# Optimization experiments

Measured on AMD Instinct MI355X. Metric: run time of the kernel, lower is better.

Reference implementation:

```python
import jax, jax.numpy as jnp
import numpy as np

N = 100000   # nodes
E = 600000   # edges
G = 4096     # graphs in batch
D_IN = 73
D_E = 101
D = 128      # latent_dim
BN_EPS = 1e-5


def _bn(h, gamma, beta):
    # BatchNorm1d in training mode: batch statistics (biased variance)
    m = h.mean(axis=0)
    v = h.var(axis=0)
    return (h - m) * jax.lax.rsqrt(v + BN_EPS) * gamma + beta


def setup_inputs() -> dict:
    key = jax.random.key(0)
    ks = jax.random.split(key, 24)
    inp = {
        "x": jax.random.normal(ks[0], (N, D_IN), jnp.float32),
        "edge_attr": jax.random.normal(ks[1], (E, D_E), jnp.float32),
        "src": jax.random.randint(ks[2], (E,), 0, N, jnp.int32),
        "dst": jax.random.randint(ks[3], (E,), 0, N, jnp.int32),
        "batch": jnp.sort(jax.random.randint(ks[4], (N,), 0, G, jnp.int32)),
        # node embedding Linear(73 -> 128)
        "W_emb": jax.random.normal(ks[5], (D_IN, D), jnp.float32) / np.sqrt(D_IN),
        "b_emb": jnp.zeros((D,), jnp.float32),
    }
    k = 6
    for i in range(2):
        inp[f"We{i}"] = jax.random.normal(ks[k], (D_E, D), jnp.float32) / np.sqrt(D_E); k += 1
        inp[f"be{i}"] = jnp.zeros((D,), jnp.float32)
        inp[f"W1_{i}"] = jax.random.normal(ks[k], (D, 2 * D), jnp.float32) / np.sqrt(D); k += 1
        inp[f"b1_{i}"] = jnp.zeros((2 * D,), jnp.float32)
        inp[f"g1_{i}"] = jnp.ones((2 * D,), jnp.float32)
        inp[f"bb1_{i}"] = jnp.zeros((2 * D,), jnp.float32)
        inp[f"W2_{i}"] = jax.random.normal(ks[k], (2 * D, D), jnp.float32) / np.sqrt(2 * D); k += 1
        inp[f"b2_{i}"] = jnp.zeros((D,), jnp.float32)
        inp[f"go_{i}"] = jnp.ones((D,), jnp.float32)
        inp[f"bo_{i}"] = jnp.zeros((D,), jnp.float32)
    return inp


def _forward(x, edge_attr, src, dst, batch,
             W_emb, b_emb,
             We0, be0, W1_0, b1_0, g1_0, bb1_0, W2_0, b2_0, go_0, bo_0,
             We1, be1, W1_1, b1_1, g1_1, bb1_1, W2_1, b2_1, go_1, bo_1):
    layers = [
        (We0, be0, W1_0, b1_0, g1_0, bb1_0, W2_0, b2_0, go_0, bo_0),
        (We1, be1, W1_1, b1_1, g1_1, bb1_1, W2_1, b2_1, go_1, bo_1),
    ]
    h = x @ W_emb + b_emb  # [N, D]
    n_layers = len(layers)
    for i, (We, be, W1, b1, g1, bb1, W2, b2, go, bo) in enumerate(layers):
        e = edge_attr @ We + be                         # [E, D]
        msg = jax.nn.relu(h[src] + e)                   # gather + add + ReLU
        agg = jax.ops.segment_sum(msg, dst, num_segments=N)  # scatter-sum
        z = h + agg                                     # (1 + eps) * x_i + aggr, eps = 0
        z = jax.nn.relu(_bn(z @ W1 + b1, g1, bb1))      # MLP: Linear -> BN -> ReLU
        h = _bn(z @ W2 + b2, go, bo)                    # Linear -> outer BN
        if i != n_layers - 1:
            h = jax.nn.relu(h)
        # dropout p=0 -> identity
    # global mean pool over graphs
    sums = jax.ops.segment_sum(h, batch, num_segments=G)            # [G, D]
    counts = jax.ops.segment_sum(jnp.ones((h.shape[0],), h.dtype), batch, num_segments=G)
    return sums / jnp.maximum(counts, 1.0)[:, None]


def reference(x, edge_attr, src, dst, batch,
              W_emb, b_emb,
              We0, be0, W1_0, b1_0, g1_0, bb1_0, W2_0, b2_0, go_0, bo_0,
              We1, be1, W1_1, b1_1, g1_1, bb1_1, W2_1, b2_1, go_1, bo_1):
    return _forward(x, edge_attr, src, dst, batch, W_emb, b_emb,
                    We0, be0, W1_0, b1_0, g1_0, bb1_0, W2_0, b2_0, go_0, bo_0,
                    We1, be1, W1_1, b1_1, g1_1, bb1_1, W2_1, b2_1, go_1, bo_1)
```

## Files before the change

### kernel.cpp

```cpp
#include <hip/hip_runtime.h>
#include <cstddef>

#define NN  100000
#define NE  600000
#define NG  4096
#define DIN 73
#define DE  101
#define DD  128
#define DD2 256
#define NP  100096
#define EP  600064

typedef unsigned int uint;
typedef unsigned short ushort;
typedef __attribute__((ext_vector_type(8))) short bf16x8;
typedef __attribute__((ext_vector_type(4))) float f32x4;

__device__ __forceinline__ void fadd_atomic(float* p, float v) { unsafeAtomicAdd(p, v); }

__device__ __forceinline__ ushort f2bf(float f) {
    uint u = __float_as_uint(f);
    uint r = (u + 0x7fffu + ((u >> 16) & 1u)) >> 16;
    return (ushort)r;
}
__device__ __forceinline__ float bf2f(ushort u) { return __uint_as_float(((uint)u) << 16); }


__global__ void hist_kernel(const int* __restrict__ dst, int* __restrict__ deg) {
    int e = blockIdx.x * blockDim.x + threadIdx.x;
    if (e < NE) atomicAdd(&deg[dst[e]], 1);
}

__global__ __launch_bounds__(256) void scan_chunk_kernel(
    const int* __restrict__ deg, int* __restrict__ offs, int* __restrict__ csums)
{
    const int b = blockIdx.x, t = threadIdx.x;
    const int base = b * 1024 + t * 4;
    int v[4];
    #pragma unroll
    for (int i = 0; i < 4; ++i) v[i] = (base + i < NN) ? deg[base + i] : 0;
    int tsum = v[0] + v[1] + v[2] + v[3];
    const int lane = t & 63, w = t >> 6;
    int x = tsum;
    #pragma unroll
    for (int d = 1; d < 64; d <<= 1) {
        int y = __shfl_up(x, d, 64);
        if (lane >= d) x += y;
    }
    __shared__ int wsum[4];
    if (lane == 63) wsum[w] = x;
    __syncthreads();
    int woff = 0;
    for (int i = 0; i < w; ++i) woff += wsum[i];
    int run = woff + x - tsum;
    #pragma unroll
    for (int i = 0; i < 4; ++i) {
        if (base + i < NN) offs[base + i] = run;
        run += v[i];
    }
    if (t == 255) csums[b] = woff + x;
}

__global__ void scan_tops_kernel(int* __restrict__ csums, int* __restrict__ offs, int nchunks) {
    if (threadIdx.x == 0 && blockIdx.x == 0) {
        int run = 0;
        for (int i = 0; i < nchunks; ++i) { int c = csums[i]; csums[i] = run; run += c; }
        offs[NN] = run;
    }
}

__global__ void scan_add_kernel(int* __restrict__ offs, const int* __restrict__ csums) {
    int i = blockIdx.x * blockDim.x + threadIdx.x;
    if (i < NN) offs[i] += csums[i >> 10];
}

__global__ void scatter_kernel(const int* __restrict__ dst, const int* __restrict__ src,
                               const int* __restrict__ offs, int* __restrict__ cursor,
                               int* __restrict__ eperm, int* __restrict__ srcp)
{
    int e = blockIdx.x * blockDim.x + threadIdx.x;
    if (e >= NE) return;
    int d = dst[e];
    int pos = offs[d] + atomicAdd(&cursor[d], 1);
    eperm[e] = pos;
    srcp[pos] = src[e];
}

__global__ void gstart_kernel(const int* __restrict__ batch, int* __restrict__ gstart) {
    int n = blockIdx.x * blockDim.x + threadIdx.x;
    if (n > NN) return;
    if (n == NN) {
        for (int g = batch[NN - 1] + 1; g <= NG; ++g) gstart[g] = NN;
        return;
    }
    int b = batch[n];
    int pb = (n == 0) ? -1 : batch[n - 1];
    for (int g = pb + 1; g <= b; ++g) gstart[g] = n;
}


__global__ __launch_bounds__(256) void cvt_ea_kernel(const float* __restrict__ ea,
                                                     const int* __restrict__ eperm,
                                                     ushort* __restrict__ eabc)
{
    const int t = threadIdx.x;
    const int r = blockIdx.x * 8 + (t >> 5);
    if (r >= NE) return;
    const int pos = eperm[r];
    const int c = (t & 31) * 4;
    ushort4 o;
    #pragma unroll
    for (int i = 0; i < 4; ++i) {
        const int col = c + i;
        float v = (col < DE) ? ea[(size_t)r * DE + col] : ((col == DE) ? 1.0f : 0.0f);
        ((ushort*)&o)[i] = f2bf(v);
    }
    *(ushort4*)&eabc[(size_t)pos * 128 + c] = o;
}

__global__ void cvt_wt_kernel(const float* __restrict__ in, ushort* __restrict__ out,
                              int Kin, int Nn, int Kp, const float* __restrict__ bias)
{
    const int n = blockIdx.x;
    for (int k = threadIdx.x; k < Kp; k += blockDim.x) {
        float v = 0.0f;
        if (k < Kin) v = in[(size_t)k * Nn + n];
        else if (k == Kin && bias) v = bias[n];
        out[(size_t)n * Kp + k] = f2bf(v);
    }
}


__global__ __launch_bounds__(256, 2) void edge_gemm_kernel(
    const ushort* __restrict__ eab, const ushort* __restrict__ Wt,
    ushort* __restrict__ ecsr)
{
    const int wid = threadIdx.x >> 6;
    const int msub = wid >> 1, nsl = wid & 1;
    const int lane = threadIdx.x & 63, l15 = lane & 15, grp = lane >> 4;
    const int n0 = nsl * 64;
    bf16x8 A[4][4];
    #pragma unroll
    for (int nf = 0; nf < 4; ++nf)
        #pragma unroll
        for (int kk = 0; kk < 4; ++kk)
            A[nf][kk] = *(const bf16x8*)(Wt + (size_t)(n0 + nf * 16 + l15) * 128 + kk * 32 + grp * 8);

    const int ntiles = EP / 128;
    for (int t = blockIdx.x; t < ntiles; t += gridDim.x) {
        const int m0 = t * 128 + msub * 64;
        f32x4 acc[4][4];
        #pragma unroll
        for (int i = 0; i < 4; ++i)
            #pragma unroll
            for (int j = 0; j < 4; ++j) acc[i][j] = (f32x4){0.f, 0.f, 0.f, 0.f};
        #pragma unroll
        for (int kk = 0; kk < 4; ++kk) {
            bf16x8 b[4];
            #pragma unroll
            for (int mf = 0; mf < 4; ++mf)
                b[mf] = *(const bf16x8*)(eab + (size_t)(m0 + mf * 16 + l15) * 128 + kk * 32 + grp * 8);
            #pragma unroll
            for (int mf = 0; mf < 4; ++mf)
                #pragma unroll
                for (int nf = 0; nf < 4; ++nf)
                    acc[mf][nf] = __builtin_amdgcn_mfma_f32_16x16x32_bf16(A[nf][kk], b[mf], acc[mf][nf], 0, 0, 0);
        }
        #pragma unroll
        for (int mf = 0; mf < 4; ++mf) {
            ushort* rp = &ecsr[(size_t)(m0 + mf * 16 + l15) * 128 + n0];
            #pragma unroll
            for (int nf = 0; nf < 4; ++nf) {
                ushort4 o;
                o.x = f2bf(acc[mf][nf][0]);
                o.y = f2bf(acc[mf][nf][1]);
                o.z = f2bf(acc[mf][nf][2]);
                o.w = f2bf(acc[mf][nf][3]);
                *(ushort4*)&rp[nf * 16 + grp * 4] = o;
            }
        }
    }
}

__global__ __launch_bounds__(256, 2) void mlp1_gemm_kernel(
    const ushort* __restrict__ z, const ushort* __restrict__ Wt,
    const float* __restrict__ bias, ushort* __restrict__ y)
{
    const int n0 = (threadIdx.x >> 6) * 64;
    const int lane = threadIdx.x & 63, l15 = lane & 15, grp = lane >> 4;
    bf16x8 A[4][4];
    #pragma unroll
    for (int nf = 0; nf < 4; ++nf)
        #pragma unroll
        for (int kk = 0; kk < 4; ++kk)
            A[nf][kk] = *(const bf16x8*)(Wt + (size_t)(n0 + nf * 16 + l15) * 128 + kk * 32 + grp * 8);
    float4 bv[4];
    #pragma unroll
    for (int nf = 0; nf < 4; ++nf) bv[nf] = *(const float4*)&bias[n0 + nf * 16 + grp * 4];

    const int ntiles = NP / 64;
    for (int t = blockIdx.x; t < ntiles; t += gridDim.x) {
        const int m0 = t * 64;
        f32x4 acc[4][4];
        #pragma unroll
        for (int i = 0; i < 4; ++i)
            #pragma unroll
            for (int j = 0; j < 4; ++j) acc[i][j] = (f32x4){0.f, 0.f, 0.f, 0.f};
        #pragma unroll
        for (int kk = 0; kk < 4; ++kk) {
            bf16x8 b[4];
            #pragma unroll
            for (int mf = 0; mf < 4; ++mf)
                b[mf] = *(const bf16x8*)(z + (size_t)(m0 + mf * 16 + l15) * 128 + kk * 32 + grp * 8);
            #pragma unroll
            for (int mf = 0; mf < 4; ++mf)
                #pragma unroll
                for (int nf = 0; nf < 4; ++nf)
                    acc[mf][nf] = __builtin_amdgcn_mfma_f32_16x16x32_bf16(A[nf][kk], b[mf], acc[mf][nf], 0, 0, 0);
        }
        #pragma unroll
        for (int mf = 0; mf < 4; ++mf) {
            ushort* rp = &y[(size_t)(m0 + mf * 16 + l15) * 256 + n0];
            #pragma unroll
            for (int nf = 0; nf < 4; ++nf) {
                ushort4 o;
                o.x = f2bf(acc[mf][nf][0] + bv[nf].x);
                o.y = f2bf(acc[mf][nf][1] + bv[nf].y);
                o.z = f2bf(acc[mf][nf][2] + bv[nf].z);
                o.w = f2bf(acc[mf][nf][3] + bv[nf].w);
                *(ushort4*)&rp[nf * 16 + grp * 4] = o;
            }
        }
    }
}

__global__ __launch_bounds__(256, 2) void mlp2_gemm_kernel(
    const ushort* __restrict__ y1, const ushort* __restrict__ Wt,
    const float* __restrict__ bias, ushort* __restrict__ y2)
{
    const int wid = threadIdx.x >> 6;
    const int msub = wid >> 1, nsl = wid & 1;
    const int lane = threadIdx.x & 63, l15 = lane & 15, grp = lane >> 4;
    const int n0 = nsl * 64;
    bf16x8 A[4][8];
    #pragma unroll
    for (int nf = 0; nf < 4; ++nf)
        #pragma unroll
        for (int kk = 0; kk < 8; ++kk)
            A[nf][kk] = *(const bf16x8*)(Wt + (size_t)(n0 + nf * 16 + l15) * 256 + kk * 32 + grp * 8);
    float4 bv[4];
    #pragma unroll
    for (int nf = 0; nf < 4; ++nf) bv[nf] = *(const float4*)&bias[n0 + nf * 16 + grp * 4];

    const int ntiles = NP / 128;
    for (int t = blockIdx.x; t < ntiles; t += gridDim.x) {
        const int m0 = t * 128 + msub * 64;
        f32x4 acc[4][4];
        #pragma unroll
        for (int i = 0; i < 4; ++i)
            #pragma unroll
            for (int j = 0; j < 4; ++j) acc[i][j] = (f32x4){0.f, 0.f, 0.f, 0.f};
        #pragma unroll
        for (int kk = 0; kk < 8; ++kk) {
            bf16x8 b[4];
            #pragma unroll
            for (int mf = 0; mf < 4; ++mf)
                b[mf] = *(const bf16x8*)(y1 + (size_t)(m0 + mf * 16 + l15) * 256 + kk * 32 + grp * 8);
            #pragma unroll
            for (int mf = 0; mf < 4; ++mf)
                #pragma unroll
                for (int nf = 0; nf < 4; ++nf)
                    acc[mf][nf] = __builtin_amdgcn_mfma_f32_16x16x32_bf16(A[nf][kk], b[mf], acc[mf][nf], 0, 0, 0);
        }
        #pragma unroll
        for (int mf = 0; mf < 4; ++mf) {
            ushort* rp = &y2[(size_t)(m0 + mf * 16 + l15) * 128 + n0];
            #pragma unroll
            for (int nf = 0; nf < 4; ++nf) {
                ushort4 o;
                o.x = f2bf(acc[mf][nf][0] + bv[nf].x);
                o.y = f2bf(acc[mf][nf][1] + bv[nf].y);
                o.z = f2bf(acc[mf][nf][2] + bv[nf].z);
                o.w = f2bf(acc[mf][nf][3] + bv[nf].w);
                *(ushort4*)&rp[nf * 16 + grp * 4] = o;
            }
        }
    }
}


__global__ __launch_bounds__(128) void embed_kernel(
    const float* __restrict__ x, const float* __restrict__ W,
    const float* __restrict__ b, ushort* __restrict__ hb)
{
    __shared__ float xs[4][DIN];
    const int n0 = blockIdx.x * 4;
    const int d  = threadIdx.x;
    for (int idx = d; idx < 4 * DIN; idx += 128) {
        int r = idx / DIN, c = idx - r * DIN;
        xs[r][c] = x[(size_t)n0 * DIN + idx];
    }
    __syncthreads();
    float bb = b[d];
    float a0 = bb, a1 = bb, a2 = bb, a3 = bb;
    for (int k = 0; k < DIN; ++k) {
        float w = W[k * DD + d];
        a0 = fmaf(xs[0][k], w, a0);
        a1 = fmaf(xs[1][k], w, a1);
        a2 = fmaf(xs[2][k], w, a2);
        a3 = fmaf(xs[3][k], w, a3);
    }
    hb[(size_t)(n0 + 0) * DD + d] = f2bf(a0);
    hb[(size_t)(n0 + 1) * DD + d] = f2bf(a1);
    hb[(size_t)(n0 + 2) * DD + d] = f2bf(a2);
    hb[(size_t)(n0 + 3) * DD + d] = f2bf(a3);
}

__global__ __launch_bounds__(256) void agg_kernel(
    const int* __restrict__ offs, const int* __restrict__ srcp,
    const ushort* __restrict__ ecsr, const ushort* __restrict__ hb,
    ushort* __restrict__ zb)
{
    const int n = blockIdx.x * 4 + (threadIdx.x >> 6);
    if (n >= NN) return;
    const int lane = threadIdx.x & 63;
    const int s = offs[n], t = offs[n + 1];
    float a0 = 0.f, a1 = 0.f;
    for (int i = s; i < t; ++i) {
        const int sp = srcp[i];
        const uint ev = *(const uint*)&ecsr[(size_t)i * 128 + lane * 2];
        const uint hv = *(const uint*)&hb[(size_t)sp * 128 + lane * 2];
        a0 += fmaxf(__uint_as_float(ev << 16) + __uint_as_float(hv << 16), 0.f);
        a1 += fmaxf(__uint_as_float(ev & 0xffff0000u) + __uint_as_float(hv & 0xffff0000u), 0.f);
    }
    const uint hh = *(const uint*)&hb[(size_t)n * 128 + lane * 2];
    ushort2 o;
    o.x = f2bf(__uint_as_float(hh << 16) + a0);
    o.y = f2bf(__uint_as_float(hh & 0xffff0000u) + a1);
    *(ushort2*)&zb[(size_t)n * 128 + lane * 2] = o;
}

__global__ __launch_bounds__(256) void colstats256_kernel(
    const ushort* __restrict__ y, float* __restrict__ s, float* __restrict__ q)
{
    const int t = threadIdx.x;
    const int cs = (t & 63) * 4, rg = t >> 6;
    const int r0 = blockIdx.x * 256;
    float ps0 = 0, ps1 = 0, ps2 = 0, ps3 = 0, pq0 = 0, pq1 = 0, pq2 = 0, pq3 = 0;
    for (int i = rg; i < 256; i += 4) {
        const int r = r0 + i;
        if (r >= NN) break;
        ushort4 u = *(const ushort4*)&y[(size_t)r * 256 + cs];
        float f0 = bf2f(u.x), f1 = bf2f(u.y), f2v = bf2f(u.z), f3 = bf2f(u.w);
        ps0 += f0; pq0 += f0 * f0;
        ps1 += f1; pq1 += f1 * f1;
        ps2 += f2v; pq2 += f2v * f2v;
        ps3 += f3; pq3 += f3 * f3;
    }
    __shared__ float SS[4][256], SQ[4][256];
    SS[rg][cs + 0] = ps0; SS[rg][cs + 1] = ps1; SS[rg][cs + 2] = ps2; SS[rg][cs + 3] = ps3;
    SQ[rg][cs + 0] = pq0; SQ[rg][cs + 1] = pq1; SQ[rg][cs + 2] = pq2; SQ[rg][cs + 3] = pq3;
    __syncthreads();
    if (rg == 0) {
        #pragma unroll
        for (int j = 0; j < 4; ++j) {
            const int c = cs + j;
            fadd_atomic(&s[c], SS[0][c] + SS[1][c] + SS[2][c] + SS[3][c]);
            fadd_atomic(&q[c], SQ[0][c] + SQ[1][c] + SQ[2][c] + SQ[3][c]);
        }
    }
}

__global__ __launch_bounds__(256) void colstats128b_kernel(
    const ushort* __restrict__ y, float* __restrict__ s, float* __restrict__ q)
{
    const int t = threadIdx.x;
    const int cs = (t & 31) * 4, rg = t >> 5;
    const int r0 = blockIdx.x * 256;
    float ps0 = 0, ps1 = 0, ps2 = 0, ps3 = 0, pq0 = 0, pq1 = 0, pq2 = 0, pq3 = 0;
    for (int i = rg; i < 256; i += 8) {
        const int r = r0 + i;
        if (r >= NN) break;
        ushort4 u = *(const ushort4*)&y[(size_t)r * 128 + cs];
        float f0 = bf2f(u.x), f1 = bf2f(u.y), f2v = bf2f(u.z), f3 = bf2f(u.w);
        ps0 += f0; pq0 += f0 * f0;
        ps1 += f1; pq1 += f1 * f1;
        ps2 += f2v; pq2 += f2v * f2v;
        ps3 += f3; pq3 += f3 * f3;
    }
    __shared__ float SS[8][128], SQ[8][128];
    SS[rg][cs + 0] = ps0; SS[rg][cs + 1] = ps1; SS[rg][cs + 2] = ps2; SS[rg][cs + 3] = ps3;
    SQ[rg][cs + 0] = pq0; SQ[rg][cs + 1] = pq1; SQ[rg][cs + 2] = pq2; SQ[rg][cs + 3] = pq3;
    __syncthreads();
    if (rg == 0) {
        #pragma unroll
        for (int j = 0; j < 4; ++j) {
            const int c = cs + j;
            float sv = 0, qv = 0;
            #pragma unroll
            for (int g = 0; g < 8; ++g) { sv += SS[g][c]; qv += SQ[g][c]; }
            fadd_atomic(&s[c], sv);
            fadd_atomic(&q[c], qv);
        }
    }
}

__global__ void finalize_kernel(const float* __restrict__ s, const float* __restrict__ sq,
                                const float* __restrict__ g, const float* __restrict__ bb,
                                float* __restrict__ a, float* __restrict__ c,
                                int dim, float invN)
{
    int d = blockIdx.x * blockDim.x + threadIdx.x;
    if (d >= dim) return;
    float m  = s[d] * invN;
    float v  = sq[d] * invN - m * m;
    float rs = rsqrtf(v + 1e-5f);
    float ai = g[d] * rs;
    a[d] = ai;
    c[d] = bb[d] - m * ai;
}

__global__ void bnrelu_bf_kernel(ushort* __restrict__ y, const float* __restrict__ a,
                                 const float* __restrict__ c)
{
    int i = blockIdx.x * blockDim.x + threadIdx.x;
    const int stride = gridDim.x * blockDim.x;
    for (; i < NN * 64; i += stride) {
        const int cb = (i & 63) * 4;
        ushort4 u = *(const ushort4*)&y[(size_t)i * 4];
        const float4 av = *(const float4*)&a[cb];
        const float4 cv = *(const float4*)&c[cb];
        ushort4 o;
        o.x = f2bf(fmaxf(fmaf(bf2f(u.x), av.x, cv.x), 0.f));
        o.y = f2bf(fmaxf(fmaf(bf2f(u.y), av.y, cv.y), 0.f));
        o.z = f2bf(fmaxf(fmaf(bf2f(u.z), av.z, cv.z), 0.f));
        o.w = f2bf(fmaxf(fmaf(bf2f(u.w), av.w, cv.w), 0.f));
        *(ushort4*)&y[(size_t)i * 4] = o;
    }
}

__global__ void bnrelu_hb_kernel(ushort* __restrict__ hb, const float* __restrict__ a,
                                 const float* __restrict__ c)
{
    int i = blockIdx.x * blockDim.x + threadIdx.x;
    const int stride = gridDim.x * blockDim.x;
    for (; i < NN * 32; i += stride) {
        const int cb = (i & 31) * 4;
        ushort4 u = *(const ushort4*)&hb[(size_t)i * 4];
        const float4 av = *(const float4*)&a[cb];
        const float4 cv = *(const float4*)&c[cb];
        ushort4 o;
        o.x = f2bf(fmaxf(fmaf(bf2f(u.x), av.x, cv.x), 0.f));
        o.y = f2bf(fmaxf(fmaf(bf2f(u.y), av.y, cv.y), 0.f));
        o.z = f2bf(fmaxf(fmaf(bf2f(u.z), av.z, cv.z), 0.f));
        o.w = f2bf(fmaxf(fmaf(bf2f(u.w), av.w, cv.w), 0.f));
        *(ushort4*)&hb[(size_t)i * 4] = o;
    }
}

__global__ __launch_bounds__(256) void pool_kernel(
    const ushort* __restrict__ hb, const float* __restrict__ a2, const float* __restrict__ c2,
    const int* __restrict__ gstart, float* __restrict__ out)
{
    const int g = blockIdx.x * 4 + (threadIdx.x >> 6);
    if (g >= NG) return;
    const int lane = threadIdx.x & 63;
    const int s = gstart[g], t = gstart[g + 1];
    float a0 = 0.f, a1 = 0.f;
    for (int n = s; n < t; ++n) {
        const uint v = *(const uint*)&hb[(size_t)n * 128 + lane * 2];
        a0 += __uint_as_float(v << 16);
        a1 += __uint_as_float(v & 0xffff0000u);
    }
    const int d0 = lane * 2;
    float2 o;
    if (t > s) {
        const float inv = 1.0f / (float)(t - s);
        o.x = fmaf(a2[d0 + 0], a0 * inv, c2[d0 + 0]);
        o.y = fmaf(a2[d0 + 1], a1 * inv, c2[d0 + 1]);
    } else {
        o.x = 0.f; o.y = 0.f;
    }
    *(float2*)&out[(size_t)g * 128 + d0] = o;
}


extern "C" void kernel_launch(void* const* d_in, const int* in_sizes, int n_in,
                              void* d_out, int out_size, void* d_ws, size_t ws_size,
                              hipStream_t stream)
{
    (void)in_sizes; (void)n_in; (void)out_size; (void)ws_size;
    const float* x     = (const float*)d_in[0];
    const float* ea    = (const float*)d_in[1];
    const int*   src   = (const int*)d_in[2];
    const int*   dst   = (const int*)d_in[3];
    const int*   batch = (const int*)d_in[4];
    const float* W_emb = (const float*)d_in[5];
    const float* b_emb = (const float*)d_in[6];

    char* ws = (char*)d_ws;
    auto alloc = [&](size_t bytes) { void* p = ws; ws += (bytes + 255) & ~(size_t)255; return p; };

    ushort* hb   = (ushort*)alloc((size_t)NP * 128 * 2);
    ushort* zb   = (ushort*)alloc((size_t)NP * 128 * 2);
    ushort* eabc = (ushort*)alloc((size_t)EP * 128 * 2);
    ushort* big  = (ushort*)alloc((size_t)EP * 128 * 2);
    ushort* ecsr = big;
    ushort* y1b  = big;
    int* deg    = (int*)alloc((size_t)NN * 4);
    int* offs   = (int*)alloc((size_t)(NN + 1) * 4);
    int* eperm  = (int*)alloc((size_t)NE * 4);
    int* srcp   = (int*)alloc((size_t)NE * 4);
    int* csums  = (int*)alloc(128 * 4);
    int* gstart = (int*)alloc((size_t)(NG + 1) * 4);
    ushort* Wet[2], *W1t[2], *W2t[2];
    for (int l = 0; l < 2; ++l) {
        Wet[l] = (ushort*)alloc(128 * 128 * 2);
        W1t[l] = (ushort*)alloc(256 * 128 * 2);
        W2t[l] = (ushort*)alloc(128 * 256 * 2);
    }
    float* st = (float*)alloc(2048 * 4);
    float* s1 = st,        *sq1 = st + 256, *a1 = st + 512,  *c1 = st + 768;
    float* s2 = st + 1024, *sq2 = st + 1152, *a2 = st + 1280, *c2 = st + 1408;
    float* out = (float*)d_out;

    const int NCHUNK = (NN + 1023) / 1024;

    hipMemsetAsync(deg, 0, (size_t)NN * 4, stream);
    hist_kernel<<<(NE + 255) / 256, 256, 0, stream>>>(dst, deg);
    scan_chunk_kernel<<<NCHUNK, 256, 0, stream>>>(deg, offs, csums);
    scan_tops_kernel<<<1, 1, 0, stream>>>(csums, offs, NCHUNK);
    scan_add_kernel<<<(NN + 255) / 256, 256, 0, stream>>>(offs, csums);
    hipMemsetAsync(deg, 0, (size_t)NN * 4, stream);
    scatter_kernel<<<(NE + 255) / 256, 256, 0, stream>>>(dst, src, offs, deg, eperm, srcp);
    gstart_kernel<<<(NN + 256) / 256, 256, 0, stream>>>(batch, gstart);

    cvt_ea_kernel<<<(NE + 7) / 8, 256, 0, stream>>>(ea, eperm, eabc);
    for (int l = 0; l < 2; ++l) {
        const float* const* L = (const float* const*)(d_in + 7 + l * 10);
        cvt_wt_kernel<<<128, 128, 0, stream>>>(L[0], Wet[l], 101, 128, 128, L[1]);
        cvt_wt_kernel<<<256, 128, 0, stream>>>(L[2], W1t[l], 128, 256, 128, nullptr);
        cvt_wt_kernel<<<128, 128, 0, stream>>>(L[6], W2t[l], 256, 128, 256, nullptr);
    }

    embed_kernel<<<NN / 4, 128, 0, stream>>>(x, W_emb, b_emb, hb);

    for (int layer = 0; layer < 2; ++layer) {
        const float* const* L = (const float* const*)(d_in + 7 + layer * 10);
        const float* b1  = L[3];
        const float* g1  = L[4]; const float* bb1 = L[5];
        const float* b2  = L[7];
        const float* go  = L[8]; const float* bo  = L[9];

        edge_gemm_kernel<<<1172, 256, 0, stream>>>(eabc, Wet[layer], ecsr);
        agg_kernel<<<NN / 4, 256, 0, stream>>>(offs, srcp, ecsr, hb, zb);

        hipMemsetAsync(s1, 0, 512 * sizeof(float), stream);
        hipMemsetAsync(s2, 0, 256 * sizeof(float), stream);

        mlp1_gemm_kernel<<<782, 256, 0, stream>>>(zb, W1t[layer], b1, y1b);
        colstats256_kernel<<<NP / 256 + 1, 256, 0, stream>>>(y1b, s1, sq1);
        finalize_kernel<<<1, 256, 0, stream>>>(s1, sq1, g1, bb1, a1, c1, 256, 1.0f / NN);
        bnrelu_bf_kernel<<<2048, 256, 0, stream>>>(y1b, a1, c1);
        mlp2_gemm_kernel<<<391, 256, 0, stream>>>(y1b, W2t[layer], b2, hb);
        colstats128b_kernel<<<NP / 256 + 1, 256, 0, stream>>>(hb, s2, sq2);
        finalize_kernel<<<1, 128, 0, stream>>>(s2, sq2, go, bo, a2, c2, 128, 1.0f / NN);

        if (layer == 0) {
            bnrelu_hb_kernel<<<2048, 256, 0, stream>>>(hb, a2, c2);
        } else {
            pool_kernel<<<NG / 4, 256, 0, stream>>>(hb, a2, c2, gstart, out);
        }
    }
}
```

Measured before the change: 1.055 ms.

## Fuse edge GEMM with gather, ReLU and segmented atomic scatter-sum

The edge-feature GEMM now gathers h[src], adds it, applies ReLU, and reduces rows sharing a destination node within each 128-row CSR tile through LDS. Each partial sum is then atomically added into an fp32 z buffer, which a new init kernel pre-fills with h. This removes the bf16 E×128 edge-message intermediate (one write plus one read) and the separate aggregation kernel. In exchange it adds fp32 atomics, a 4x-larger fp32 z buffer that the MLP1 GEMM must now read and convert to bf16, and an extra init pass over z.

```diff
diff --git a/kernel.cpp b/kernel.cpp
--- a/kernel.cpp
+++ b/kernel.cpp
@@ -25,6 +25,17 @@
 }
 __device__ __forceinline__ float bf2f(ushort u) { return __uint_as_float(((uint)u) << 16); }
 
+__device__ __forceinline__ bf16x8 ld_zfrag(const float* __restrict__ p) {
+    const float4 f0 = *(const float4*)p;
+    const float4 f1 = *(const float4*)(p + 4);
+    bf16x8 r;
+    r[0] = (short)f2bf(f0.x); r[1] = (short)f2bf(f0.y);
+    r[2] = (short)f2bf(f0.z); r[3] = (short)f2bf(f0.w);
+    r[4] = (short)f2bf(f1.x); r[5] = (short)f2bf(f1.y);
+    r[6] = (short)f2bf(f1.z); r[7] = (short)f2bf(f1.w);
+    return r;
+}
+
 
 __global__ void hist_kernel(const int* __restrict__ dst, int* __restrict__ deg) {
     int e = blockIdx.x * blockDim.x + threadIdx.x;
@@ -76,7 +87,8 @@
 
 __global__ void scatter_kernel(const int* __restrict__ dst, const int* __restrict__ src,
                                const int* __restrict__ offs, int* __restrict__ cursor,
-                               int* __restrict__ eperm, int* __restrict__ srcp)
+                               int* __restrict__ eperm, int* __restrict__ srcp,
+                               int* __restrict__ dstp)
 {
     int e = blockIdx.x * blockDim.x + threadIdx.x;
     if (e >= NE) return;
@@ -84,6 +96,7 @@
     int pos = offs[d] + atomicAdd(&cursor[d], 1);
     eperm[e] = pos;
     srcp[pos] = src[e];
+    dstp[pos] = d;
 }
 
 __global__ void gstart_kernel(const int* __restrict__ batch, int* __restrict__ gstart) {
@@ -130,15 +143,19 @@
     }
 }
 
-
-__global__ __launch_bounds__(256, 2) void edge_gemm_kernel(
+__global__ __launch_bounds__(256, 2) void edge_agg_kernel(
     const ushort* __restrict__ eab, const ushort* __restrict__ Wt,
-    ushort* __restrict__ ecsr)
-{
-    const int wid = threadIdx.x >> 6;
+    const int* __restrict__ srcp, const int* __restrict__ dstp,
+    const ushort* __restrict__ hb, float* __restrict__ zf)
+{
+    __shared__ ushort vals[128 * 128];
+    __shared__ int nd[128];
+    const int tid = threadIdx.x;
+    const int wid = tid >> 6;
     const int msub = wid >> 1, nsl = wid & 1;
-    const int lane = threadIdx.x & 63, l15 = lane & 15, grp = lane >> 4;
+    const int lane = tid & 63, l15 = lane & 15, grp = lane >> 4;
     const int n0 = nsl * 64;
+
     bf16x8 A[4][4];
     #pragma unroll
     for (int nf = 0; nf < 4; ++nf)
@@ -146,9 +163,30 @@
         for (int kk = 0; kk < 4; ++kk)
             A[nf][kk] = *(const bf16x8*)(Wt + (size_t)(n0 + nf * 16 + l15) * 128 + kk * 32 + grp * 8);
 
+    const int rcol = tid & 127;
+    const int rh   = tid >> 7;
+
     const int ntiles = EP / 128;
     for (int t = blockIdx.x; t < ntiles; t += gridDim.x) {
-        const int m0 = t * 128 + msub * 64;
+        const int r0 = t * 128;
+        const int m0 = r0 + msub * 64;
+        __syncthreads();
+        if (tid < 128) {
+            const int rr = r0 + tid;
+            nd[tid] = (rr < NE) ? dstp[rr] : NN;
+        }
+        int sp[4];
+        #pragma unroll
+        for (int mf = 0; mf < 4; ++mf) {
+            const int rr = m0 + mf * 16 + l15;
+            sp[mf] = (rr < NE) ? srcp[rr] : 0;
+        }
+        ushort4 hv[4][4];
+        #pragma unroll
+        for (int mf = 0; mf < 4; ++mf)
+            #pragma unroll
+            for (int nf = 0; nf < 4; ++nf)
+                hv[mf][nf] = *(const ushort4*)&hb[(size_t)sp[mf] * 128 + n0 + nf * 16 + grp * 4];
         f32x4 acc[4][4];
         #pragma unroll
         for (int i = 0; i < 4; ++i)
@@ -168,22 +206,54 @@
         }
         #pragma unroll
         for (int mf = 0; mf < 4; ++mf) {
-            ushort* rp = &ecsr[(size_t)(m0 + mf * 16 + l15) * 128 + n0];
+            const int row = msub * 64 + mf * 16 + l15;
+            const int sw = (row & 7) << 3;
             #pragma unroll
             for (int nf = 0; nf < 4; ++nf) {
+                const int col = n0 + nf * 16 + grp * 4;
                 ushort4 o;
-                o.x = f2bf(acc[mf][nf][0]);
-                o.y = f2bf(acc[mf][nf][1]);
-                o.z = f2bf(acc[mf][nf][2]);
-                o.w = f2bf(acc[mf][nf][3]);
-                *(ushort4*)&rp[nf * 16 + grp * 4] = o;
+                o.x = f2bf(fmaxf(acc[mf][nf][0] + bf2f(hv[mf][nf].x), 0.f));
+                o.y = f2bf(fmaxf(acc[mf][nf][1] + bf2f(hv[mf][nf].y), 0.f));
+                o.z = f2bf(fmaxf(acc[mf][nf][2] + bf2f(hv[mf][nf].z), 0.f));
+                o.w = f2bf(fmaxf(acc[mf][nf][3] + bf2f(hv[mf][nf].w), 0.f));
+                *(ushort4*)&vals[row * 128 + (col ^ sw)] = o;
             }
         }
-    }
-}
+        __syncthreads();
+        float accs = 0.f;
+        int cur = nd[rh * 64];
+        for (int r = rh * 64; r < rh * 64 + 64; ++r) {
+            const int node = nd[r];
+            const float v = bf2f(vals[r * 128 + (rcol ^ ((r & 7) << 3))]);
+            if (node != cur) {
+                if (cur < NN) fadd_atomic(&zf[(size_t)cur * 128 + rcol], accs);
+                accs = 0.f; cur = node;
+            }
+            accs += v;
+        }
+        if (cur < NN) fadd_atomic(&zf[(size_t)cur * 128 + rcol], accs);
+    }
+}
+
+__global__ void zinit_kernel(const ushort* __restrict__ hb, float* __restrict__ zf) {
+    int i = blockIdx.x * blockDim.x + threadIdx.x;
+    const int stride = gridDim.x * blockDim.x;
+    for (; i < NP * 32; i += stride) {
+        const int n = i >> 5;
+        float4 o;
+        if (n < NN) {
+            ushort4 u = *(const ushort4*)&hb[(size_t)i * 4];
+            o.x = bf2f(u.x); o.y = bf2f(u.y); o.z = bf2f(u.z); o.w = bf2f(u.w);
+        } else {
+            o.x = 0.f; o.y = 0.f; o.z = 0.f; o.w = 0.f;
+        }
+        *(float4*)&zf[(size_t)i * 4] = o;
+    }
+}
+
 
 __global__ __launch_bounds__(256, 2) void mlp1_gemm_kernel(
-    const ushort* __restrict__ z, const ushort* __restrict__ Wt,
+    const float* __restrict__ z, const ushort* __restrict__ Wt,
     const float* __restrict__ bias, ushort* __restrict__ y)
 {
     const int n0 = (threadIdx.x >> 6) * 64;
@@ -211,7 +281,7 @@
             bf16x8 b[4];
             #pragma unroll
             for (int mf = 0; mf < 4; ++mf)
-                b[mf] = *(const bf16x8*)(z + (size_t)(m0 + mf * 16 + l15) * 128 + kk * 32 + grp * 8);
+                b[mf] = ld_zfrag(z + (size_t)(m0 + mf * 16 + l15) * 128 + kk * 32 + grp * 8);
             #pragma unroll
             for (int mf = 0; mf < 4; ++mf)
                 #pragma unroll
@@ -314,30 +384,6 @@
     hb[(size_t)(n0 + 1) * DD + d] = f2bf(a1);
     hb[(size_t)(n0 + 2) * DD + d] = f2bf(a2);
     hb[(size_t)(n0 + 3) * DD + d] = f2bf(a3);
-}
-
-__global__ __launch_bounds__(256) void agg_kernel(
-    const int* __restrict__ offs, const int* __restrict__ srcp,
-    const ushort* __restrict__ ecsr, const ushort* __restrict__ hb,
-    ushort* __restrict__ zb)
-{
-    const int n = blockIdx.x * 4 + (threadIdx.x >> 6);
-    if (n >= NN) return;
-    const int lane = threadIdx.x & 63;
-    const int s = offs[n], t = offs[n + 1];
-    float a0 = 0.f, a1 = 0.f;
-    for (int i = s; i < t; ++i) {
-        const int sp = srcp[i];
-        const uint ev = *(const uint*)&ecsr[(size_t)i * 128 + lane * 2];
-        const uint hv = *(const uint*)&hb[(size_t)sp * 128 + lane * 2];
-        a0 += fmaxf(__uint_as_float(ev << 16) + __uint_as_float(hv << 16), 0.f);
-        a1 += fmaxf(__uint_as_float(ev & 0xffff0000u) + __uint_as_float(hv & 0xffff0000u), 0.f);
-    }
-    const uint hh = *(const uint*)&hb[(size_t)n * 128 + lane * 2];
-    ushort2 o;
-    o.x = f2bf(__uint_as_float(hh << 16) + a0);
-    o.y = f2bf(__uint_as_float(hh & 0xffff0000u) + a1);
-    *(ushort2*)&zb[(size_t)n * 128 + lane * 2] = o;
 }
 
 __global__ __launch_bounds__(256) void colstats256_kernel(
@@ -502,15 +548,14 @@
     auto alloc = [&](size_t bytes) { void* p = ws; ws += (bytes + 255) & ~(size_t)255; return p; };
 
     ushort* hb   = (ushort*)alloc((size_t)NP * 128 * 2);
-    ushort* zb   = (ushort*)alloc((size_t)NP * 128 * 2);
+    float*  zf   = (float*) alloc((size_t)NP * 128 * 4);
     ushort* eabc = (ushort*)alloc((size_t)EP * 128 * 2);
-    ushort* big  = (ushort*)alloc((size_t)EP * 128 * 2);
-    ushort* ecsr = big;
-    ushort* y1b  = big;
+    ushort* y1b  = (ushort*)alloc((size_t)NP * 256 * 2);
     int* deg    = (int*)alloc((size_t)NN * 4);
     int* offs   = (int*)alloc((size_t)(NN + 1) * 4);
     int* eperm  = (int*)alloc((size_t)NE * 4);
     int* srcp   = (int*)alloc((size_t)NE * 4);
+    int* dstp   = (int*)alloc((size_t)NE * 4);
     int* csums  = (int*)alloc(128 * 4);
     int* gstart = (int*)alloc((size_t)(NG + 1) * 4);
     ushort* Wet[2], *W1t[2], *W2t[2];
@@ -532,7 +577,7 @@
     scan_tops_kernel<<<1, 1, 0, stream>>>(csums, offs, NCHUNK);
     scan_add_kernel<<<(NN + 255) / 256, 256, 0, stream>>>(offs, csums);
     hipMemsetAsync(deg, 0, (size_t)NN * 4, stream);
-    scatter_kernel<<<(NE + 255) / 256, 256, 0, stream>>>(dst, src, offs, deg, eperm, srcp);
+    scatter_kernel<<<(NE + 255) / 256, 256, 0, stream>>>(dst, src, offs, deg, eperm, srcp, dstp);
     gstart_kernel<<<(NN + 256) / 256, 256, 0, stream>>>(batch, gstart);
 
     cvt_ea_kernel<<<(NE + 7) / 8, 256, 0, stream>>>(ea, eperm, eabc);
@@ -552,13 +597,13 @@
         const float* b2  = L[7];
         const float* go  = L[8]; const float* bo  = L[9];
 
-        edge_gemm_kernel<<<1172, 256, 0, stream>>>(eabc, Wet[layer], ecsr);
-        agg_kernel<<<NN / 4, 256, 0, stream>>>(offs, srcp, ecsr, hb, zb);
+        zinit_kernel<<<2048, 256, 0, stream>>>(hb, zf);
+        edge_agg_kernel<<<1172, 256, 0, stream>>>(eabc, Wet[layer], srcp, dstp, hb, zf);
 
         hipMemsetAsync(s1, 0, 512 * sizeof(float), stream);
         hipMemsetAsync(s2, 0, 256 * sizeof(float), stream);
 
-        mlp1_gemm_kernel<<<782, 256, 0, stream>>>(zb, W1t[layer], b1, y1b);
+        mlp1_gemm_kernel<<<782, 256, 0, stream>>>(zf, W1t[layer], b1, y1b);
         colstats256_kernel<<<NP / 256 + 1, 256, 0, stream>>>(y1b, s1, sq1);
         finalize_kernel<<<1, 256, 0, stream>>>(s1, sq1, g1, bb1, a1, c1, 256, 1.0f / NN);
         bnrelu_bf_kernel<<<2048, 256, 0, stream>>>(y1b, a1, c1);
```

Result: no change. 1.039 ms (-1.6%).
